# Kernel tuning notes

Measured on AMD Instinct MI355X. Metric: run time of the kernel, lower is better.

Reference implementation:

```python
import jax, jax.numpy as jnp
import numpy as np

N_QUBITS = 9
C64 = jnp.complex64

PZ = jnp.array([[1, 0], [0, -1]], dtype=C64)
PX = jnp.array([[0, 1], [1, 0]], dtype=C64)
PY = jnp.array([[0, -1j], [1j, 0]], dtype=C64)
CNOT = jnp.array([[1, 0, 0, 0], [0, 1, 0, 0], [0, 0, 0, 1], [0, 0, 1, 0]], dtype=C64).reshape(2, 2, 2, 2)


def _rx(t):
    c = jnp.cos(t / 2).astype(C64)
    s = jnp.sin(t / 2).astype(C64)
    return jnp.stack([jnp.stack([c, -1j * s]), jnp.stack([-1j * s, c])])


def _ry(t):
    c = jnp.cos(t / 2).astype(C64)
    s = jnp.sin(t / 2).astype(C64)
    return jnp.stack([jnp.stack([c, -s]), jnp.stack([s, c])])


def _ap1(state, g, q):
    # apply 2x2 gate g on qubit axis q of state with shape (2,)*n
    return jnp.moveaxis(jnp.tensordot(g, state, axes=((1,), (q,))), 0, q)


def _ap2(state, g, q1, q2):
    return jnp.moveaxis(jnp.tensordot(g, state, axes=((2, 3), (q1, q2))), (0, 1), (q1, q2))


def _simulate(x, w, n, Denc, D):
    state = jnp.zeros((2,) * n, dtype=C64).at[(0,) * n].set(1.0)
    idx = 0
    for j in range(n):
        state = _ap1(state, _rx(x[idx]), j)
        state = _ap1(state, _ry(x[idx + 1]), j)
        idx += 2
    for _ in range(Denc):
        for j in range(n):
            state = _ap2(state, CNOT, j, (j + 1) % n)
        for j in range(n):
            state = _ap1(state, _ry(x[idx]), j)
            idx += 1
    idx = 0
    for j in range(n):
        state = _ap1(state, _rx(w[idx]), j)
        state = _ap1(state, _ry(w[idx + 1]), j)
        idx += 2
    for _ in range(D):
        for j in range(n):
            state = _ap2(state, CNOT, j, (j + 1) % n)
        for j in range(n):
            state = _ap1(state, _ry(w[idx]), j)
            idx += 1
    return state


def _expZ0(state):
    return jnp.real(jnp.vdot(state, _ap1(state, PZ, 0)))


def _expvals(state, n, ngroups):
    # E[p, q] = <Pauli_p on qubit q>; observable i -> qubit i%n, pauli (i//n)%3 (Z,X,Y)
    E = jnp.stack([jnp.stack([jnp.real(jnp.vdot(state, _ap1(state, P, q))) for q in range(n)])
                   for P in (PZ, PX, PY)])
    return jnp.concatenate([E[g % 3] for g in range(ngroups)])


def _forward(inp, wq, wk, wv):
    B, S, d = inp.shape
    n = N_QUBITS
    Denc = d // n - 2
    D = wq.shape[0] // n - 2
    flat = jnp.swapaxes(inp, 0, 1).reshape(S * B, d)  # matches torch transpose(0,1).reshape
    qk_fn = jax.vmap(lambda x, w: _expZ0(_simulate(x, w, n, Denc, D)), in_axes=(0, None))
    v_fn = jax.vmap(lambda x: _expvals(_simulate(x, wv, n, Denc, D), n, Denc + 2))
    Q = qk_fn(flat, wq).reshape(S, B, 1).swapaxes(0, 1).astype(inp.dtype)  # (B,S,1)
    K = qk_fn(flat, wk).reshape(S, B, 1).swapaxes(0, 1).astype(inp.dtype)
    V = v_fn(flat).reshape(S, B, d).swapaxes(0, 1).astype(inp.dtype)       # (B,S,d)
    alpha = jnp.exp(-(Q[:, :, None, :] - K[:, None, :, :]) ** 2)  # (B,S,S,1)
    alpha = alpha / jnp.sum(alpha, axis=2, keepdims=True)
    return inp + jnp.sum(alpha * V[:, None, :, :], axis=2)


def setup_inputs() -> dict:
    key = jax.random.key(0)
    k1, k2, k3, k4 = jax.random.split(key, 4)
    B, S, n, Denc, D = 48, 96, 9, 4, 8
    d = n * (Denc + 2)          # 54
    wdim = n * (D + 2)          # 90
    pi4 = np.float32(np.pi / 4)
    return {
        "input": jax.random.normal(k1, (B, S, d), dtype=jnp.float32),
        "params_Q": pi4 * (2 * jax.random.normal(k2, (wdim,), dtype=jnp.float32) - 1),
        "params_K": pi4 * (2 * jax.random.normal(k3, (wdim,), dtype=jnp.float32) - 1),
        "params_V": pi4 * (2 * jax.random.normal(k4, (wdim,), dtype=jnp.float32) - 1),
    }


def reference(input, params_Q, params_K, params_V):
    return _forward(input, params_Q, params_K, params_V)
```

## Files before the change

### kernel.cpp

```cpp
#include <hip/hip_runtime.h>
#include <math.h>

#define B_DIM  48
#define S_DIM  96
#define D_DIM  54
#define DENC   4
#define DVAR   8
#define NFLAT  (B_DIM * S_DIM)

typedef _Float16 h2 __attribute__((ext_vector_type(2)));

__device__ __forceinline__ int h2i(h2 v) { return __builtin_bit_cast(int, v); }
__device__ __forceinline__ h2  i2h(int v) { return __builtin_bit_cast(h2, v); }

template<int LM>
__device__ __forceinline__ int lxi(int x, int lane) {
    if constexpr (LM == 1)       return __builtin_amdgcn_update_dpp(x, x, 0xB1, 0xF, 0xF, true);
    else if constexpr (LM == 2)  return __builtin_amdgcn_update_dpp(x, x, 0x4E, 0xF, 0xF, true);
    else if constexpr (LM == 4)  return __builtin_amdgcn_ds_swizzle(x, 0x101F);
    else if constexpr (LM == 8)  return __builtin_amdgcn_update_dpp(x, x, 0x128, 0xF, 0xF, true);
    else if constexpr (LM == 16) return __builtin_amdgcn_ds_swizzle(x, 0x401F);
    else {
        auto r = __builtin_amdgcn_permlane32_swap(x, x, false, false);
        return (lane & 32) ? r[0] : r[1];
    }
}
template<int LM>
__device__ __forceinline__ float lx(float v, int lane) {
    return __int_as_float(lxi<LM>(__float_as_int(v), lane));
}

__device__ __forceinline__ float wave_sum(float v, int lane) {
    v += lx<32>(v, lane);
    v += lx<16>(v, lane);
    v += lx<8>(v, lane);
    v += lx<4>(v, lane);
    v += lx<2>(v, lane);
    v += lx<1>(v, lane);
    return v;
}


__device__ __forceinline__ h2 hswap(h2 v) {
    int p = h2i(v);
    return i2h(__builtin_amdgcn_alignbit(p, p, 16));
}

__device__ __forceinline__ void ring(h2 st[8], int lane) {
    const int gray = (lane ^ (lane >> 1)) << 2;
#pragma unroll
    for (int r = 0; r < 8; ++r)
        st[r] = i2h(__builtin_amdgcn_ds_bpermute(gray, h2i(st[r])));
    {
        const bool c0 = (lane & 1) != 0;
#pragma unroll
        for (int r = 0; r < 4; ++r) {
            h2 a = st[r], b = st[r + 4];
            st[r]     = c0 ? b : a;
            st[r + 4] = c0 ? a : b;
        }
    }
    { h2 t = st[4]; st[4] = st[6]; st[6] = t; }
    { h2 t = st[5]; st[5] = st[7]; st[7] = t; }
    { h2 t = st[2]; st[2] = st[3]; st[3] = t; }
    { h2 t = st[6]; st[6] = st[7]; st[7] = t; }
#pragma unroll
    for (int r = 1; r < 8; r += 2)
        st[r] = i2h(lxi<32>(h2i(st[r]), lane));
}

template<int BJ>
__device__ __forceinline__ void rot_ry(h2 st[8], int c2i, int s2i, int lane) {
    const h2 c2 = i2h(c2i);
    if constexpr (BJ >= 3) {
        constexpr int lm = 1 << (BJ - 3);
        const h2 sg = i2h((lane & lm) ? s2i : (s2i ^ 0x80008000));
#pragma unroll
        for (int r = 0; r < 8; ++r) {
            h2 p = i2h(lxi<lm>(h2i(st[r]), lane));
            st[r] = st[r] * c2 + p * sg;
        }
    } else {
        constexpr int M = 1 << BJ;
        const h2 s2 = i2h(s2i), ns2 = i2h(s2i ^ 0x80008000);
#pragma unroll
        for (int r = 0; r < 8; ++r) {
            if ((r & M) == 0) {
                h2 a = st[r], b = st[r + M];
                st[r]     = a * c2 + b * ns2;
                st[r + M] = b * c2 + a * s2;
            }
        }
    }
}

template<int BJ>
__device__ __forceinline__ void rot_rx(h2 st[8], int c2i, int s2i, int lane) {
    const h2 c2 = i2h(c2i);
    const h2 sm = i2h(s2i ^ 0x80000000);
    if constexpr (BJ >= 3) {
        constexpr int lm = 1 << (BJ - 3);
#pragma unroll
        for (int r = 0; r < 8; ++r) {
            h2 p = i2h(lxi<lm>(h2i(st[r]), lane));
            st[r] = st[r] * c2 + hswap(p) * sm;
        }
    } else {
        constexpr int M = 1 << BJ;
#pragma unroll
        for (int r = 0; r < 8; ++r) {
            if ((r & M) == 0) {
                h2 a = st[r], b = st[r + M];
                st[r]     = a * c2 + hswap(b) * sm;
                st[r + M] = b * c2 + hswap(a) * sm;
            }
        }
    }
}

#define INITQ(j) { rot_rx<8 - (j)>(st, cc[2 * (j)],     ss[2 * (j)],     lane);  \
                   rot_ry<8 - (j)>(st, cc[2 * (j) + 1], ss[2 * (j) + 1], lane); }

__device__ __forceinline__ void run_circuit(h2 st[8], const int* cc, const int* ss,
                                            int layers, int lane) {
    INITQ(0) INITQ(1) INITQ(2) INITQ(3) INITQ(4)
    INITQ(5) INITQ(6) INITQ(7) INITQ(8)
    const int* pc = cc + 18;
    const int* ps = ss + 18;
#pragma unroll 1
    for (int L = 0; L < layers; ++L) {
        ring(st, lane);
        rot_ry<8>(st, pc[0], ps[0], lane);
        rot_ry<7>(st, pc[1], ps[1], lane);
        rot_ry<6>(st, pc[2], ps[2], lane);
        rot_ry<5>(st, pc[3], ps[3], lane);
        rot_ry<4>(st, pc[4], ps[4], lane);
        rot_ry<3>(st, pc[5], ps[5], lane);
        rot_ry<2>(st, pc[6], ps[6], lane);
        rot_ry<1>(st, pc[7], ps[7], lane);
        rot_ry<0>(st, pc[8], ps[8], lane);
        pc += 9; ps += 9;
    }
}

template<int BJ>
__device__ __forceinline__ void expv(const h2 st[8], int lane, float& ez, float& ex, float& ey) {
    ez = ex = ey = 0.f;
    if constexpr (BJ >= 3) {
        constexpr int lm = 1 << (BJ - 3);
        const float sgn = (lane & lm) ? -1.f : 1.f;
#pragma unroll
        for (int r = 0; r < 8; ++r) {
            h2 p = i2h(lxi<lm>(h2i(st[r]), lane));
            float x = (float)st[r].x, y = (float)st[r].y;
            float px = (float)p.x,   py = (float)p.y;
            ez += sgn * (x * x + y * y);
            ex += x * px + y * py;
            ey += sgn * (x * py - y * px);
        }
    } else {
        constexpr int M = 1 << BJ;
#pragma unroll
        for (int r = 0; r < 8; ++r) {
            if ((r & M) == 0) {
                float ax = (float)st[r].x,     ay = (float)st[r].y;
                float bx = (float)st[r + M].x, by = (float)st[r + M].y;
                ez += (ax * ax + ay * ay) - (bx * bx + by * by);
                ex += 2.f * (ax * bx + ay * by);
                ey += 2.f * (ax * by - ay * bx);
            }
        }
    }
    ez = wave_sum(ez, lane); ex = wave_sum(ex, lane); ey = wave_sum(ey, lane);
}

__global__ __launch_bounds__(64) void sim_kernel(
    const float* __restrict__ inp, const float* __restrict__ wq,
    const float* __restrict__ wk,  const float* __restrict__ wv,
    float* __restrict__ outQ, float* __restrict__ outK, float* __restrict__ outV)
{
    __shared__ int csc[324];
    __shared__ int css[324];

    const int lane = threadIdx.x;
    const int fi   = blockIdx.x;
    const int b = fi % B_DIM, s = fi / B_DIM;
    const float* x = inp + ((size_t)b * S_DIM + s) * D_DIM;

    for (int k = lane; k < 324; k += 64) {
        float ang = (k < 54)  ? x[k]
                  : (k < 144) ? wq[k - 54]
                  : (k < 234) ? wk[k - 144]
                              : wv[k - 234];
        float sn, cn; sincosf(0.5f * ang, &sn, &cn);
        _Float16 hc = (_Float16)cn, hs = (_Float16)sn;
        h2 c2 = {hc, hc}, s2 = {hs, hs};
        csc[k] = h2i(c2);
        css[k] = h2i(s2);
    }

    h2 st[8], ck[8];
#pragma unroll
    for (int r = 0; r < 8; ++r) st[r] = i2h(0);
    if (lane == 0) { h2 one = {(_Float16)1.f, (_Float16)0.f}; st[0] = one; }

    run_circuit(st, csc, css, DENC, lane);
#pragma unroll
    for (int r = 0; r < 8; ++r) ck[r] = st[r];

    run_circuit(st, csc + 54, css + 54, DVAR, lane);
    {
        float p = 0.f;
#pragma unroll
        for (int r = 0; r < 8; ++r) {
            float xx = (float)st[r].x, yy = (float)st[r].y;
            p += xx * xx + yy * yy;
        }
        p = (lane & 32) ? -p : p;
        p = wave_sum(p, lane);
        if (lane == 0) outQ[fi] = p;
    }

#pragma unroll
    for (int r = 0; r < 8; ++r) st[r] = ck[r];
    run_circuit(st, csc + 144, css + 144, DVAR, lane);
    {
        float p = 0.f;
#pragma unroll
        for (int r = 0; r < 8; ++r) {
            float xx = (float)st[r].x, yy = (float)st[r].y;
            p += xx * xx + yy * yy;
        }
        p = (lane & 32) ? -p : p;
        p = wave_sum(p, lane);
        if (lane == 0) outK[fi] = p;
    }

#pragma unroll
    for (int r = 0; r < 8; ++r) st[r] = ck[r];
    run_circuit(st, csc + 234, css + 234, DVAR, lane);
    {
        float* vrow = outV + (size_t)fi * D_DIM;
#define EXPQ(q) { float ez, ex, ey; expv<8 - (q)>(st, lane, ez, ex, ey);            \
                  if (lane == 0) { vrow[(q)] = ez; vrow[9 + (q)] = ex;              \
                                   vrow[18 + (q)] = ey; vrow[27 + (q)] = ez;        \
                                   vrow[36 + (q)] = ex; vrow[45 + (q)] = ey; } }
        EXPQ(0) EXPQ(1) EXPQ(2) EXPQ(3) EXPQ(4)
        EXPQ(5) EXPQ(6) EXPQ(7) EXPQ(8)
#undef EXPQ
    }
}

__global__ __launch_bounds__(256) void attn_kernel(
    const float* __restrict__ inp, const float* __restrict__ Q,
    const float* __restrict__ K,   const float* __restrict__ V,
    float* __restrict__ out)
{
    __shared__ float w4[4][S_DIM];
    const int warp = threadIdx.x >> 6;
    const int t    = threadIdx.x & 63;
    const int bi   = blockIdx.x * 4 + warp;
    const int b    = bi / S_DIM;
    const int i    = bi % S_DIM;
    float* w = w4[warp];

    const float q = Q[i * B_DIM + b];
    float e0, e1 = 0.f;
    {
        float d0 = q - K[t * B_DIM + b];
        e0 = expf(-d0 * d0);
        w[t] = e0;
        if (t < S_DIM - 64) {
            float d1 = q - K[(t + 64) * B_DIM + b];
            e1 = expf(-d1 * d1);
            w[t + 64] = e1;
        }
    }
    float ps = wave_sum(e0 + e1, t);
    const float inv = 1.f / ps;

    if (t < D_DIM) {
        float acc = 0.f;
        for (int j = 0; j < S_DIM; ++j)
            acc += w[j] * V[(size_t)(j * B_DIM + b) * D_DIM + t];
        size_t o = (size_t)bi * D_DIM + t;
        out[o] = inp[o] + acc * inv;
    }
}

extern "C" void kernel_launch(void* const* d_in, const int* in_sizes, int n_in,
                              void* d_out, int out_size, void* d_ws, size_t ws_size,
                              hipStream_t stream)
{
    (void)in_sizes; (void)n_in; (void)out_size; (void)ws_size;
    const float* inp = (const float*)d_in[0];
    const float* wq  = (const float*)d_in[1];
    const float* wk  = (const float*)d_in[2];
    const float* wv  = (const float*)d_in[3];
    float* outp = (float*)d_out;

    float* Qw = (float*)d_ws;
    float* Kw = Qw + NFLAT;
    float* Vw = Kw + NFLAT;

    sim_kernel<<<NFLAT, 64, 0, stream>>>(inp, wq, wk, wv, Qw, Kw, Vw);
    attn_kernel<<<NFLAT / 4, 256, 0, stream>>>(inp, Qw, Kw, Vw, outp);
}
```

Before: 109.5 us.

## Interleave Q, K, V variational circuits in one wave for ILP

Instead of running the Q, K and V variational circuits one after another from the shared encoded state, the kernel now keeps three state vectors in registers and applies each gate to all three together. This interleaves independent DPP, swizzle and bpermute lane exchanges and FMAs so their latencies can overlap inside one wave. The cost is roughly three times the state registers (24 packed half2 values plus three sets of coefficients), which can lower occupancy or cause spills.

```diff
diff --git a/kernel.cpp b/kernel.cpp
--- a/kernel.cpp
+++ b/kernel.cpp
@@ -46,11 +46,7 @@
     return i2h(__builtin_amdgcn_alignbit(p, p, 16));
 }
 
-__device__ __forceinline__ void ring(h2 st[8], int lane) {
-    const int gray = (lane ^ (lane >> 1)) << 2;
-#pragma unroll
-    for (int r = 0; r < 8; ++r)
-        st[r] = i2h(__builtin_amdgcn_ds_bpermute(gray, h2i(st[r])));
+__device__ __forceinline__ void ring_tail(h2 st[8], int lane) {
     {
         const bool c0 = (lane & 1) != 0;
 #pragma unroll
@@ -69,77 +65,77 @@
         st[r] = i2h(lxi<32>(h2i(st[r]), lane));
 }
 
-template<int BJ>
-__device__ __forceinline__ void rot_ry(h2 st[8], int c2i, int s2i, int lane) {
-    const h2 c2 = i2h(c2i);
+template<int NP>
+__device__ __forceinline__ void ringN(h2 st[][8], int lane) {
+    const int gray = (lane ^ (lane >> 1)) << 2;
+#pragma unroll
+    for (int r = 0; r < 8; ++r)
+#pragma unroll
+        for (int p = 0; p < NP; ++p)
+            st[p][r] = i2h(__builtin_amdgcn_ds_bpermute(gray, h2i(st[p][r])));
+#pragma unroll
+    for (int p = 0; p < NP; ++p)
+        ring_tail(st[p], lane);
+}
+
+template<int NP, int BJ>
+__device__ __forceinline__ void rot_ryN(h2 st[][8], const int* c2, const int* s2, int lane) {
     if constexpr (BJ >= 3) {
         constexpr int lm = 1 << (BJ - 3);
-        const h2 sg = i2h((lane & lm) ? s2i : (s2i ^ 0x80008000));
-#pragma unroll
-        for (int r = 0; r < 8; ++r) {
-            h2 p = i2h(lxi<lm>(h2i(st[r]), lane));
-            st[r] = st[r] * c2 + p * sg;
+        int sg[NP];
+#pragma unroll
+        for (int p = 0; p < NP; ++p) sg[p] = (lane & lm) ? s2[p] : (s2[p] ^ 0x80008000);
+#pragma unroll
+        for (int r = 0; r < 8; ++r) {
+#pragma unroll
+            for (int p = 0; p < NP; ++p) {
+                h2 pt = i2h(lxi<lm>(h2i(st[p][r]), lane));
+                st[p][r] = st[p][r] * i2h(c2[p]) + pt * i2h(sg[p]);
+            }
         }
     } else {
         constexpr int M = 1 << BJ;
-        const h2 s2 = i2h(s2i), ns2 = i2h(s2i ^ 0x80008000);
 #pragma unroll
         for (int r = 0; r < 8; ++r) {
             if ((r & M) == 0) {
-                h2 a = st[r], b = st[r + M];
-                st[r]     = a * c2 + b * ns2;
-                st[r + M] = b * c2 + a * s2;
-            }
-        }
-    }
-}
-
-template<int BJ>
-__device__ __forceinline__ void rot_rx(h2 st[8], int c2i, int s2i, int lane) {
-    const h2 c2 = i2h(c2i);
-    const h2 sm = i2h(s2i ^ 0x80000000);
+#pragma unroll
+                for (int p = 0; p < NP; ++p) {
+                    h2 a = st[p][r], b = st[p][r + M];
+                    h2 c2h = i2h(c2[p]), s2h = i2h(s2[p]), ns2h = i2h(s2[p] ^ 0x80008000);
+                    st[p][r]     = a * c2h + b * ns2h;
+                    st[p][r + M] = b * c2h + a * s2h;
+                }
+            }
+        }
+    }
+}
+
+template<int NP, int BJ>
+__device__ __forceinline__ void rot_rxN(h2 st[][8], const int* c2, const int* s2, int lane) {
     if constexpr (BJ >= 3) {
         constexpr int lm = 1 << (BJ - 3);
 #pragma unroll
         for (int r = 0; r < 8; ++r) {
-            h2 p = i2h(lxi<lm>(h2i(st[r]), lane));
-            st[r] = st[r] * c2 + hswap(p) * sm;
+#pragma unroll
+            for (int p = 0; p < NP; ++p) {
+                h2 pt = i2h(lxi<lm>(h2i(st[p][r]), lane));
+                st[p][r] = st[p][r] * i2h(c2[p]) + hswap(pt) * i2h(s2[p] ^ 0x80000000);
+            }
         }
     } else {
         constexpr int M = 1 << BJ;
 #pragma unroll
         for (int r = 0; r < 8; ++r) {
             if ((r & M) == 0) {
-                h2 a = st[r], b = st[r + M];
-                st[r]     = a * c2 + hswap(b) * sm;
-                st[r + M] = b * c2 + hswap(a) * sm;
-            }
-        }
-    }
-}
-
-#define INITQ(j) { rot_rx<8 - (j)>(st, cc[2 * (j)],     ss[2 * (j)],     lane);  \
-                   rot_ry<8 - (j)>(st, cc[2 * (j) + 1], ss[2 * (j) + 1], lane); }
-
-__device__ __forceinline__ void run_circuit(h2 st[8], const int* cc, const int* ss,
-                                            int layers, int lane) {
-    INITQ(0) INITQ(1) INITQ(2) INITQ(3) INITQ(4)
-    INITQ(5) INITQ(6) INITQ(7) INITQ(8)
-    const int* pc = cc + 18;
-    const int* ps = ss + 18;
-#pragma unroll 1
-    for (int L = 0; L < layers; ++L) {
-        ring(st, lane);
-        rot_ry<8>(st, pc[0], ps[0], lane);
-        rot_ry<7>(st, pc[1], ps[1], lane);
-        rot_ry<6>(st, pc[2], ps[2], lane);
-        rot_ry<5>(st, pc[3], ps[3], lane);
-        rot_ry<4>(st, pc[4], ps[4], lane);
-        rot_ry<3>(st, pc[5], ps[5], lane);
-        rot_ry<2>(st, pc[6], ps[6], lane);
-        rot_ry<1>(st, pc[7], ps[7], lane);
-        rot_ry<0>(st, pc[8], ps[8], lane);
-        pc += 9; ps += 9;
+#pragma unroll
+                for (int p = 0; p < NP; ++p) {
+                    h2 a = st[p][r], b = st[p][r + M];
+                    h2 c2h = i2h(c2[p]), sm = i2h(s2[p] ^ 0x80000000);
+                    st[p][r]     = a * c2h + hswap(b) * sm;
+                    st[p][r + M] = b * c2h + hswap(a) * sm;
+                }
+            }
+        }
     }
 }
 
@@ -199,49 +195,89 @@
         css[k] = h2i(s2);
     }
 
-    h2 st[8], ck[8];
-#pragma unroll
-    for (int r = 0; r < 8; ++r) st[r] = i2h(0);
-    if (lane == 0) { h2 one = {(_Float16)1.f, (_Float16)0.f}; st[0] = one; }
-
-    run_circuit(st, csc, css, DENC, lane);
-#pragma unroll
-    for (int r = 0; r < 8; ++r) ck[r] = st[r];
-
-    run_circuit(st, csc + 54, css + 54, DVAR, lane);
+    h2 st[3][8];
+#pragma unroll
+    for (int r = 0; r < 8; ++r) st[0][r] = i2h(0);
+    if (lane == 0) { h2 one = {(_Float16)1.f, (_Float16)0.f}; st[0][0] = one; }
+
+#define EINIT(j) { int c1[1] = {csc[2*(j)]},     s1[1] = {css[2*(j)]};      \
+                   rot_rxN<1, 8-(j)>(st, c1, s1, lane);                     \
+                   int c1b[1] = {csc[2*(j)+1]},  s1b[1] = {css[2*(j)+1]};   \
+                   rot_ryN<1, 8-(j)>(st, c1b, s1b, lane); }
+    EINIT(0) EINIT(1) EINIT(2) EINIT(3) EINIT(4)
+    EINIT(5) EINIT(6) EINIT(7) EINIT(8)
+#undef EINIT
+    {
+        const int* pc = csc + 18;
+        const int* ps = css + 18;
+#pragma unroll 1
+        for (int L = 0; L < DENC; ++L) {
+            ringN<1>(st, lane);
+#define ERY(i, BJ) { int c1[1] = {pc[i]}, s1[1] = {ps[i]}; rot_ryN<1, BJ>(st, c1, s1, lane); }
+            ERY(0, 8) ERY(1, 7) ERY(2, 6) ERY(3, 5) ERY(4, 4)
+            ERY(5, 3) ERY(6, 2) ERY(7, 1) ERY(8, 0)
+#undef ERY
+            pc += 9; ps += 9;
+        }
+    }
+
+#pragma unroll
+    for (int r = 0; r < 8; ++r) { st[1][r] = st[0][r]; st[2][r] = st[0][r]; }
+
+    {
+        const int* cq = csc + 54;  const int* sq_ = css + 54;
+        const int* ck_ = csc + 144; const int* sk_ = css + 144;
+        const int* cv = csc + 234; const int* sv_ = css + 234;
+#define VINIT(j) { int c3[3] = {cq[2*(j)],   ck_[2*(j)],   cv[2*(j)]};      \
+                   int s3[3] = {sq_[2*(j)],  sk_[2*(j)],   sv_[2*(j)]};     \
+                   rot_rxN<3, 8-(j)>(st, c3, s3, lane);                     \
+                   int c3b[3] = {cq[2*(j)+1], ck_[2*(j)+1], cv[2*(j)+1]};   \
+                   int s3b[3] = {sq_[2*(j)+1], sk_[2*(j)+1], sv_[2*(j)+1]}; \
+                   rot_ryN<3, 8-(j)>(st, c3b, s3b, lane); }
+        VINIT(0) VINIT(1) VINIT(2) VINIT(3) VINIT(4)
+        VINIT(5) VINIT(6) VINIT(7) VINIT(8)
+#undef VINIT
+        const int* pcq = cq + 18;  const int* psq = sq_ + 18;
+        const int* pck = ck_ + 18; const int* psk = sk_ + 18;
+        const int* pcv = cv + 18;  const int* psv = sv_ + 18;
+#pragma unroll 1
+        for (int L = 0; L < DVAR; ++L) {
+            ringN<3>(st, lane);
+#define VRY(i, BJ) { int c3[3] = {pcq[i], pck[i], pcv[i]};                  \
+                     int s3[3] = {psq[i], psk[i], psv[i]};                  \
+                     rot_ryN<3, BJ>(st, c3, s3, lane); }
+            VRY(0, 8) VRY(1, 7) VRY(2, 6) VRY(3, 5) VRY(4, 4)
+            VRY(5, 3) VRY(6, 2) VRY(7, 1) VRY(8, 0)
+#undef VRY
+            pcq += 9; psq += 9; pck += 9; psk += 9; pcv += 9; psv += 9;
+        }
+    }
+
     {
         float p = 0.f;
 #pragma unroll
         for (int r = 0; r < 8; ++r) {
-            float xx = (float)st[r].x, yy = (float)st[r].y;
+            float xx = (float)st[0][r].x, yy = (float)st[0][r].y;
             p += xx * xx + yy * yy;
         }
         p = (lane & 32) ? -p : p;
         p = wave_sum(p, lane);
         if (lane == 0) outQ[fi] = p;
     }
-
-#pragma unroll
-    for (int r = 0; r < 8; ++r) st[r] = ck[r];
-    run_circuit(st, csc + 144, css + 144, DVAR, lane);
     {
         float p = 0.f;
 #pragma unroll
         for (int r = 0; r < 8; ++r) {
-            float xx = (float)st[r].x, yy = (float)st[r].y;
+            float xx = (float)st[1][r].x, yy = (float)st[1][r].y;
             p += xx * xx + yy * yy;
         }
         p = (lane & 32) ? -p : p;
         p = wave_sum(p, lane);
         if (lane == 0) outK[fi] = p;
     }
-
-#pragma unroll
-    for (int r = 0; r < 8; ++r) st[r] = ck[r];
-    run_circuit(st, csc + 234, css + 234, DVAR, lane);
     {
         float* vrow = outV + (size_t)fi * D_DIM;
-#define EXPQ(q) { float ez, ex, ey; expv<8 - (q)>(st, lane, ez, ex, ey);            \
+#define EXPQ(q) { float ez, ex, ey; expv<8 - (q)>(st[2], lane, ez, ex, ey);         \
                   if (lane == 0) { vrow[(q)] = ez; vrow[9 + (q)] = ex;              \
                                    vrow[18 + (q)] = ey; vrow[27 + (q)] = ez;        \
                                    vrow[36 + (q)] = ex; vrow[45 + (q)] = ey; } }
```

Result: no change. 108.9 us (-0.5%).
